# Kernel tuning notes

Hardware: AMD Instinct MI355X
Metric: run time of the kernel (lower is better)

## Reference

```python
import jax, jax.numpy as jnp
import numpy as np

EMBED = 1024
HEADS = 16
HEAD_SIZE = EMBED // HEADS  # 64

def setup_inputs() -> dict:
    key = jax.random.key(0)
    kx, kq, kk, kv = jax.random.split(key, 4)
    x = jax.random.normal(kx, (8, 2048, EMBED), dtype=jnp.float32)
    s = 1.0 / np.sqrt(EMBED)
    Wq = jax.random.normal(kq, (EMBED, HEAD_SIZE), dtype=jnp.float32) * s
    Wk = jax.random.normal(kk, (EMBED, HEAD_SIZE), dtype=jnp.float32) * s
    Wv = jax.random.normal(kv, (EMBED, HEAD_SIZE), dtype=jnp.float32) * s
    return {"x": x, "Wq": Wq, "Wk": Wk, "Wv": Wv}

def reference(x, Wq, Wk, Wv):
    # x: [B, S, E]; projections to [B, S, D] with D = head_size
    q = jnp.einsum('bse,ed->bsd', x, Wq)
    k = jnp.einsum('bse,ed->bsd', x, Wk)
    v = jnp.einsum('bse,ed->bsd', x, Wv)
    scale = k.shape[-1] ** -0.5
    scores = jnp.einsum('bqd,bkd->bqk', q, k) * scale  # [B, S, S]
    S = x.shape[1]
    causal = jnp.tril(jnp.ones((S, S), dtype=bool))
    scores = jnp.where(causal, scores, -jnp.inf)
    weights = jax.nn.softmax(scores, axis=-1)
    # dropout is identity in eval/reference mode
    out = jnp.einsum('bqk,bkd->bqd', weights, v)  # [B, S, D]
    return out
```

## Files before the change

kernel.cpp:

```cpp
#include <hip/hip_runtime.h>


#define BATCH 8
#define SEQ   2048
#define EMB   1024
#define HD    64
#define QBLK  16
#define NSPL  8

typedef __attribute__((ext_vector_type(8))) short short8;
typedef __attribute__((ext_vector_type(4))) short short4v;
typedef __attribute__((ext_vector_type(4))) float f32x4;

static __device__ __forceinline__ short f2bf(float f) {
    union { float f; unsigned int i; } c;
    c.f = f;
    unsigned int r = c.i + 0x7fff + ((c.i >> 16) & 1);
    return (short)(r >> 16);
}

__global__ __launch_bounds__(256) void transpose_w(
    const float* __restrict__ Wq, const float* __restrict__ Wk,
    const float* __restrict__ Wv, short* __restrict__ Wt) {
    __shared__ short tileT[64][72];
    int bid = blockIdx.x;
    int p = bid >> 4, kt = bid & 15;
    const float* W = (p == 0) ? Wq : ((p == 1) ? Wk : Wv);
    int t = threadIdx.x;
    int k0 = kt * 64;
    int row = t >> 2, c0 = (t & 3) * 16;
    const float* src = W + (long)(k0 + row) * HD + c0;
    #pragma unroll
    for (int j = 0; j < 16; ++j)
        tileT[c0 + j][row] = f2bf(src[j]);
    __syncthreads();
    int n = t >> 2, ks = (t & 3) * 16;
    short8 o0 = *(const short8*)(&tileT[n][ks]);
    short8 o1 = *(const short8*)(&tileT[n][ks + 8]);
    *(short8*)(Wt + (long)(p * 64 + n) * EMB + k0 + ks)     = o0;
    *(short8*)(Wt + (long)(p * 64 + n) * EMB + k0 + ks + 8) = o1;
}

__global__ __launch_bounds__(512) void proj_mfma(
    const float* __restrict__ x, const short* __restrict__ Wt,
    short* __restrict__ qg, short* __restrict__ kg, short* __restrict__ vtg) {
    __shared__ short xL[64][72];
    __shared__ short wL[192][72];
    __shared__ short vL[64][72];
    int t = threadIdx.x;
    int m0 = blockIdx.x * 64;
    int w = t >> 6, l = t & 63;
    int wr = w >> 2, wc = w & 3;
    int ll = l & 15, lg = l >> 4;

    f32x4 acc[2][3] = {};

    int arow = wr * 32 + ll;
    int brow = wc * 48 + ll;
    int kcol = lg * 8;

    for (int k0 = 0; k0 < EMB; k0 += 64) {
        __syncthreads();
        {
            int row = t >> 3, c8 = (t & 7) * 8;
            const float* src = x + (long)(m0 + row) * EMB + k0 + c8;
            f32x4 a = *(const f32x4*)(src);
            f32x4 b = *(const f32x4*)(src + 4);
            short8 v;
            #pragma unroll
            for (int j = 0; j < 4; ++j) { v[j] = f2bf(a[j]); v[4 + j] = f2bf(b[j]); }
            *(short8*)(&xL[row][c8]) = v;
        }
        #pragma unroll
        for (int c = 0; c < 3; ++c) {
            int idx = c * 512 + t;
            int n = idx >> 3, c8 = idx & 7;
            short8 v = *(const short8*)(Wt + (long)n * EMB + k0 + c8 * 8);
            *(short8*)(&wL[n][c8 * 8]) = v;
        }
        __syncthreads();
        #pragma unroll
        for (int ks = 0; ks < 2; ++ks) {
            short8 af[2], bf[3];
            #pragma unroll
            for (int mi = 0; mi < 2; ++mi)
                af[mi] = *(const short8*)(&xL[arow + mi * 16][kcol + ks * 32]);
            #pragma unroll
            for (int ni = 0; ni < 3; ++ni)
                bf[ni] = *(const short8*)(&wL[brow + ni * 16][kcol + ks * 32]);
            #pragma unroll
            for (int mi = 0; mi < 2; ++mi)
                #pragma unroll
                for (int ni = 0; ni < 3; ++ni)
                    acc[mi][ni] = __builtin_amdgcn_mfma_f32_16x16x32_bf16(
                        af[mi], bf[ni], acc[mi][ni], 0, 0, 0);
        }
    }
    const float cs = 0.125f * 1.44269504088896f;
    int b  = m0 >> 11;
    int s0 = m0 & 2047;
    #pragma unroll
    for (int mi = 0; mi < 2; ++mi)
        #pragma unroll
        for (int ni = 0; ni < 3; ++ni) {
            int c = wc * 48 + ni * 16 + ll;
            int mloc = wr * 32 + mi * 16 + lg * 4;
            #pragma unroll
            for (int r = 0; r < 4; ++r) {
                float av = acc[mi][ni][r];
                if (c < 64)
                    qg[(long)(m0 + mloc + r) * HD + c] = f2bf(av * cs);
                else if (c < 128)
                    kg[(long)(m0 + mloc + r) * HD + (c - 64)] = f2bf(av);
                else
                    vL[c - 128][mloc + r] = f2bf(av);
            }
        }
    __syncthreads();
    {
        int d = t >> 3, seg = (t & 7) * 8;
        short8 vv = *(const short8*)(&vL[d][seg]);
        *(short8*)(vtg + ((long)b * HD + d) * SEQ + s0 + seg) = vv;
    }
}

__global__ __launch_bounds__(512, 4) void attn_mfma(
    const short* __restrict__ qg, const short* __restrict__ kg,
    const short* __restrict__ vtg, float* __restrict__ out) {
    __shared__ short PLA[NSPL][16][72];
    __shared__ short PLB[NSPL][16][72];
    __shared__ float pO[NSPL][16][65];
    __shared__ float pLs[NSPL][16];

    int b    = blockIdx.x & 7;
    int pair = blockIdx.x >> 3;
    int qtA = pair;
    int qtB = 127 - pair;
    int q0A = qtA * QBLK, q0B = qtB * QBLK;
    int t = threadIdx.x;
    int w = t >> 6, l = t & 63;
    int ll = l & 15, lg = l >> 4;

    const short* qb = qg + (long)b * SEQ * HD;
    const short* kb = kg + (long)b * SEQ * HD;
    const short* vb = vtg + (long)b * HD * SEQ;

    short8 qfA[2], qfB[2];
    #pragma unroll
    for (int ks = 0; ks < 2; ++ks) {
        qfA[ks] = *(const short8*)(qb + (long)(q0A + ll) * HD + ks * 32 + lg * 8);
        qfB[ks] = *(const short8*)(qb + (long)(q0B + ll) * HD + ks * 32 + lg * 8);
    }

    f32x4 accA[4] = {}, accB[4] = {};
    float psA = 0.f, psB = 0.f;

    int nkvB = q0B / 64 + 1;

    for (int kt = w; kt < nkvB; kt += NSPL) {
        int kv0 = kt * 64;
        bool maskA = (kv0 + 63) > q0A;
        bool maskB = (kv0 + 63) > q0B;

        #pragma unroll
        for (int n = 0; n < 4; ++n) {
            const short* kr = kb + (long)(kv0 + n * 16 + ll) * HD + lg * 8;
            short8 kf0 = *(const short8*)(kr);
            short8 kf1 = *(const short8*)(kr + 32);
            int kvb = kv0 + n * 16 + lg * 4;

            f32x4 sA = {};
            sA = __builtin_amdgcn_mfma_f32_16x16x32_bf16(kf0, qfA[0], sA, 0, 0, 0);
            sA = __builtin_amdgcn_mfma_f32_16x16x32_bf16(kf1, qfA[1], sA, 0, 0, 0);
            short4v pkA;
            #pragma unroll
            for (int r = 0; r < 4; ++r) {
                float p = __builtin_amdgcn_exp2f(sA[r]);
                if (maskA && (kvb + r > q0A + ll)) p = 0.f;
                psA += p;
                pkA[r] = f2bf(p);
            }
            *(short4v*)(&PLA[w][ll][n * 16 + lg * 4]) = pkA;

            f32x4 sB = {};
            sB = __builtin_amdgcn_mfma_f32_16x16x32_bf16(kf0, qfB[0], sB, 0, 0, 0);
            sB = __builtin_amdgcn_mfma_f32_16x16x32_bf16(kf1, qfB[1], sB, 0, 0, 0);
            short4v pkB;
            #pragma unroll
            for (int r = 0; r < 4; ++r) {
                float p = __builtin_amdgcn_exp2f(sB[r]);
                if (maskB && (kvb + r > q0B + ll)) p = 0.f;
                psB += p;
                pkB[r] = f2bf(p);
            }
            *(short4v*)(&PLB[w][ll][n * 16 + lg * 4]) = pkB;
        }

        #pragma unroll
        for (int ks = 0; ks < 2; ++ks) {
            short8 pfA = *(const short8*)(&PLA[w][ll][ks * 32 + lg * 8]);
            short8 pfB = *(const short8*)(&PLB[w][ll][ks * 32 + lg * 8]);
            #pragma unroll
            for (int nd = 0; nd < 4; ++nd) {
                short8 vf = *(const short8*)(vb + (long)(nd * 16 + ll) * SEQ + kv0 + ks * 32 + lg * 8);
                accA[nd] = __builtin_amdgcn_mfma_f32_16x16x32_bf16(pfA, vf, accA[nd], 0, 0, 0);
                accB[nd] = __builtin_amdgcn_mfma_f32_16x16x32_bf16(pfB, vf, accB[nd], 0, 0, 0);
            }
        }
    }

    psA += __shfl_xor(psA, 16, 64);
    psA += __shfl_xor(psA, 32, 64);
    psB += __shfl_xor(psB, 16, 64);
    psB += __shfl_xor(psB, 32, 64);

    #pragma unroll
    for (int nd = 0; nd < 4; ++nd)
        #pragma unroll
        for (int r = 0; r < 4; ++r)
            pO[w][lg * 4 + r][nd * 16 + ll] = accA[nd][r];
    if (lg == 0) pLs[w][ll] = psA;
    __syncthreads();
    {
        int q = t >> 5, d0 = (t & 31) * 2;
        float L = 0.f, o0 = 0.f, o1 = 0.f;
        #pragma unroll
        for (int w2 = 0; w2 < NSPL; ++w2) {
            L  += pLs[w2][q];
            o0 += pO[w2][q][d0];
            o1 += pO[w2][q][d0 + 1];
        }
        float inv = 1.0f / L;
        float* dst = out + (long)b * SEQ * HD + (long)(q0A + q) * HD + d0;
        dst[0] = o0 * inv; dst[1] = o1 * inv;
    }
    __syncthreads();

    #pragma unroll
    for (int nd = 0; nd < 4; ++nd)
        #pragma unroll
        for (int r = 0; r < 4; ++r)
            pO[w][lg * 4 + r][nd * 16 + ll] = accB[nd][r];
    if (lg == 0) pLs[w][ll] = psB;
    __syncthreads();
    {
        int q = t >> 5, d0 = (t & 31) * 2;
        float L = 0.f, o0 = 0.f, o1 = 0.f;
        #pragma unroll
        for (int w2 = 0; w2 < NSPL; ++w2) {
            L  += pLs[w2][q];
            o0 += pO[w2][q][d0];
            o1 += pO[w2][q][d0 + 1];
        }
        float inv = 1.0f / L;
        float* dst = out + (long)b * SEQ * HD + (long)(q0B + q) * HD + d0;
        dst[0] = o0 * inv; dst[1] = o1 * inv;
    }
}

extern "C" void kernel_launch(void* const* d_in, const int* in_sizes, int n_in,
                              void* d_out, int out_size, void* d_ws, size_t ws_size,
                              hipStream_t stream) {
    const float* x  = (const float*)d_in[0];
    const float* Wq = (const float*)d_in[1];
    const float* Wk = (const float*)d_in[2];
    const float* Wv = (const float*)d_in[3];
    float* outp = (float*)d_out;

    short* Wt  = (short*)d_ws;
    short* qg  = (short*)((char*)d_ws + 393216);
    short* kg  = (short*)((char*)d_ws + 393216 + 2097152);
    short* vtg = (short*)((char*)d_ws + 393216 + 2 * 2097152);

    transpose_w<<<48, 256, 0, stream>>>(Wq, Wk, Wv, Wt);
    proj_mfma<<<BATCH * SEQ / 64, 512, 0, stream>>>(x, Wt, qg, kg, vtg);
    attn_mfma<<<SEQ / QBLK / 2 * BATCH, 512, 0, stream>>>(qg, kg, vtg, outp);
}
```

Before: 73.53 us.

## Split projection kernel per Q/K/V output with smaller 32-row tiles

The projection kernel now launches one block per (projection, 32-row tile), giving 1536 blocks of 128 threads instead of 256 blocks of 512 threads that each computed all three projections for 64 rows. This raises block count to fill the CUs better, but each block re-reads and re-converts its x tile from fp32 for each of the three projections, tripling x global traffic and conversion work. A variable in the attention kernel was also renamed to avoid shadowing the new projection index.

```diff
diff --git a/kernel.cpp b/kernel.cpp
--- a/kernel.cpp
+++ b/kernel.cpp
@@ -41,86 +41,95 @@
     *(short8*)(Wt + (long)(p * 64 + n) * EMB + k0 + ks + 8) = o1;
 }
 
-__global__ __launch_bounds__(512) void proj_mfma(
+__global__ __launch_bounds__(128) void proj_mfma(
     const float* __restrict__ x, const short* __restrict__ Wt,
     short* __restrict__ qg, short* __restrict__ kg, short* __restrict__ vtg) {
-    __shared__ short xL[64][72];
-    __shared__ short wL[192][72];
-    __shared__ short vL[64][72];
+    __shared__ short xL[32][72];
+    __shared__ short wL[64][72];
+    __shared__ short vL[64][40];
+    int bid = blockIdx.x;
+    int p = bid >> 9;
+    int m_tile = bid & 511;
+    int m0 = m_tile * 32;
     int t = threadIdx.x;
-    int m0 = blockIdx.x * 64;
     int w = t >> 6, l = t & 63;
-    int wr = w >> 2, wc = w & 3;
     int ll = l & 15, lg = l >> 4;
 
-    f32x4 acc[2][3] = {};
-
-    int arow = wr * 32 + ll;
-    int brow = wc * 48 + ll;
+    const short* Wp = Wt + (long)p * 64 * EMB;
+
+    f32x4 acc[4] = {};
+    int arow = w * 16 + ll;
     int kcol = lg * 8;
 
     for (int k0 = 0; k0 < EMB; k0 += 64) {
         __syncthreads();
         {
-            int row = t >> 3, c8 = (t & 7) * 8;
-            const float* src = x + (long)(m0 + row) * EMB + k0 + c8;
+            int row = t >> 2, c16 = (t & 3) * 16;
+            const float* src = x + (long)(m0 + row) * EMB + k0 + c16;
             f32x4 a = *(const f32x4*)(src);
             f32x4 b = *(const f32x4*)(src + 4);
-            short8 v;
-            #pragma unroll
-            for (int j = 0; j < 4; ++j) { v[j] = f2bf(a[j]); v[4 + j] = f2bf(b[j]); }
-            *(short8*)(&xL[row][c8]) = v;
-        }
-        #pragma unroll
-        for (int c = 0; c < 3; ++c) {
-            int idx = c * 512 + t;
-            int n = idx >> 3, c8 = idx & 7;
-            short8 v = *(const short8*)(Wt + (long)n * EMB + k0 + c8 * 8);
-            *(short8*)(&wL[n][c8 * 8]) = v;
+            f32x4 c = *(const f32x4*)(src + 8);
+            f32x4 d = *(const f32x4*)(src + 12);
+            short8 v0, v1;
+            #pragma unroll
+            for (int j = 0; j < 4; ++j) {
+                v0[j] = f2bf(a[j]); v0[4 + j] = f2bf(b[j]);
+                v1[j] = f2bf(c[j]); v1[4 + j] = f2bf(d[j]);
+            }
+            *(short8*)(&xL[row][c16])     = v0;
+            *(short8*)(&xL[row][c16 + 8]) = v1;
+        }
+        #pragma unroll
+        for (int j = 0; j < 2; ++j) {
+            int idx = j * 128 + t;
+            int n = idx >> 2, seg = (idx & 3) * 16;
+            const short* src = Wp + (long)n * EMB + k0 + seg;
+            short8 v0 = *(const short8*)(src);
+            short8 v1 = *(const short8*)(src + 8);
+            *(short8*)(&wL[n][seg])     = v0;
+            *(short8*)(&wL[n][seg + 8]) = v1;
         }
         __syncthreads();
         #pragma unroll
         for (int ks = 0; ks < 2; ++ks) {
-            short8 af[2], bf[3];
-            #pragma unroll
-            for (int mi = 0; mi < 2; ++mi)
-                af[mi] = *(const short8*)(&xL[arow + mi * 16][kcol + ks * 32]);
-            #pragma unroll
-            for (int ni = 0; ni < 3; ++ni)
-                bf[ni] = *(const short8*)(&wL[brow + ni * 16][kcol + ks * 32]);
-            #pragma unroll
-            for (int mi = 0; mi < 2; ++mi)
-                #pragma unroll
-                for (int ni = 0; ni < 3; ++ni)
-                    acc[mi][ni] = __builtin_amdgcn_mfma_f32_16x16x32_bf16(
-                        af[mi], bf[ni], acc[mi][ni], 0, 0, 0);
-        }
-    }
+            short8 af = *(const short8*)(&xL[arow][kcol + ks * 32]);
+            #pragma unroll
+            for (int ni = 0; ni < 4; ++ni) {
+                short8 bf = *(const short8*)(&wL[ni * 16 + ll][kcol + ks * 32]);
+                acc[ni] = __builtin_amdgcn_mfma_f32_16x16x32_bf16(af, bf, acc[ni], 0, 0, 0);
+            }
+        }
+    }
+
     const float cs = 0.125f * 1.44269504088896f;
-    int b  = m0 >> 11;
-    int s0 = m0 & 2047;
-    #pragma unroll
-    for (int mi = 0; mi < 2; ++mi)
-        #pragma unroll
-        for (int ni = 0; ni < 3; ++ni) {
-            int c = wc * 48 + ni * 16 + ll;
-            int mloc = wr * 32 + mi * 16 + lg * 4;
-            #pragma unroll
-            for (int r = 0; r < 4; ++r) {
-                float av = acc[mi][ni][r];
-                if (c < 64)
-                    qg[(long)(m0 + mloc + r) * HD + c] = f2bf(av * cs);
-                else if (c < 128)
-                    kg[(long)(m0 + mloc + r) * HD + (c - 64)] = f2bf(av);
-                else
-                    vL[c - 128][mloc + r] = f2bf(av);
-            }
-        }
-    __syncthreads();
-    {
-        int d = t >> 3, seg = (t & 7) * 8;
-        short8 vv = *(const short8*)(&vL[d][seg]);
-        *(short8*)(vtg + ((long)b * HD + d) * SEQ + s0 + seg) = vv;
+    if (p == 0) {
+        #pragma unroll
+        for (int ni = 0; ni < 4; ++ni)
+            #pragma unroll
+            for (int r = 0; r < 4; ++r)
+                qg[(long)(m0 + w * 16 + lg * 4 + r) * HD + ni * 16 + ll] =
+                    f2bf(acc[ni][r] * cs);
+    } else if (p == 1) {
+        #pragma unroll
+        for (int ni = 0; ni < 4; ++ni)
+            #pragma unroll
+            for (int r = 0; r < 4; ++r)
+                kg[(long)(m0 + w * 16 + lg * 4 + r) * HD + ni * 16 + ll] =
+                    f2bf(acc[ni][r]);
+    } else {
+        #pragma unroll
+        for (int ni = 0; ni < 4; ++ni)
+            #pragma unroll
+            for (int r = 0; r < 4; ++r)
+                vL[ni * 16 + ll][w * 16 + lg * 4 + r] = f2bf(acc[ni][r]);
+        __syncthreads();
+        int b  = m0 >> 11;
+        int s0 = m0 & 2047;
+        int d = t >> 1, seg = (t & 1) * 16;
+        short8 v0 = *(const short8*)(&vL[d][seg]);
+        short8 v1 = *(const short8*)(&vL[d][seg + 8]);
+        *(short8*)(vtg + ((long)b * HD + d) * SEQ + s0 + seg)     = v0;
+        *(short8*)(vtg + ((long)b * HD + d) * SEQ + s0 + seg + 8) = v1;
     }
 }
 
@@ -175,10 +184,10 @@
             short4v pkA;
             #pragma unroll
             for (int r = 0; r < 4; ++r) {
-                float p = __builtin_amdgcn_exp2f(sA[r]);
-                if (maskA && (kvb + r > q0A + ll)) p = 0.f;
-                psA += p;
-                pkA[r] = f2bf(p);
+                float pv = __builtin_amdgcn_exp2f(sA[r]);
+                if (maskA && (kvb + r > q0A + ll)) pv = 0.f;
+                psA += pv;
+                pkA[r] = f2bf(pv);
             }
             *(short4v*)(&PLA[w][ll][n * 16 + lg * 4]) = pkA;
 
@@ -188,10 +197,10 @@
             short4v pkB;
             #pragma unroll
             for (int r = 0; r < 4; ++r) {
-                float p = __builtin_amdgcn_exp2f(sB[r]);
-                if (maskB && (kvb + r > q0B + ll)) p = 0.f;
-                psB += p;
-                pkB[r] = f2bf(p);
+                float pv = __builtin_amdgcn_exp2f(sB[r]);
+                if (maskB && (kvb + r > q0B + ll)) pv = 0.f;
+                psB += pv;
+                pkB[r] = f2bf(pv);
             }
             *(short4v*)(&PLB[w][ll][n * 16 + lg * 4]) = pkB;
         }
@@ -273,6 +282,6 @@
     short* vtg = (short*)((char*)d_ws + 393216 + 2 * 2097152);
 
     transpose_w<<<48, 256, 0, stream>>>(Wq, Wk, Wv, Wt);
-    proj_mfma<<<BATCH * SEQ / 64, 512, 0, stream>>>(x, Wt, qg, kg, vtg);
+    proj_mfma<<<3 * 512, 128, 0, stream>>>(x, Wt, qg, kg, vtg);
     attn_mfma<<<SEQ / QBLK / 2 * BATCH, 512, 0, stream>>>(qg, kg, vtg, outp);
 }
```

Result: faster. 61.36 us (-16.5%).
